# Performance work log

Hardware: AMD Instinct MI355X
Metric: run time of the kernel (lower is better)

The kernel has to match this reference:

```python
import jax, jax.numpy as jnp
import numpy as np

B, T, L, D, H = 4, 8, 197, 512, 8
DK = D // H
SIM_TH = 0.0
N = T * (L - 1)  # 1568 local tokens

def _ln(x, g, b, eps=1e-5):
    x32 = x.astype(jnp.float32)
    m = jnp.mean(x32, axis=-1, keepdims=True)
    v = jnp.mean((x32 - m) ** 2, axis=-1, keepdims=True)
    return (((x32 - m) * jax.lax.rsqrt(v + eps)) * g + b).astype(x.dtype)

def _qgelu(x):
    return x * jax.nn.sigmoid(1.702 * x)

def _mha(x, w_in, b_in, w_out, b_out):
    # torch nn.MultiheadAttention, x: [S, Bt, D] (seq-first)
    S, Bt, _ = x.shape
    qkv = x @ w_in.T + b_in
    q, k, v = jnp.split(qkv, 3, axis=-1)
    q = q.reshape(S, Bt, H, DK); k = k.reshape(S, Bt, H, DK); v = v.reshape(S, Bt, H, DK)
    scores = jnp.einsum('sbhd,tbhd->bhst', q, k) / jnp.sqrt(jnp.asarray(DK, x.dtype))
    p = jax.nn.softmax(scores, axis=-1)
    o = jnp.einsum('bhst,tbhd->sbhd', p, v).reshape(S, Bt, D)
    return o @ w_out.T + b_out

def _resblock(x, ln1g, ln1b, inw, inb, outw, outb, ln2g, ln2b, fcw, fcb, pw, pb):
    x = x + _mha(_ln(x, ln1g, ln1b), inw, inb, outw, outb)
    h = _qgelu(_ln(x, ln2g, ln2b) @ fcw.T + fcb)
    return x + h @ pw.T + pb

def _build_graph(x, g_mask):
    xd = jax.lax.stop_gradient(x)  # matches x.detach()
    xn = xd / jnp.maximum(jnp.linalg.norm(xd, axis=-1, keepdims=True), 1e-12)
    sim = jnp.einsum('bnd,bmd->bnm', xn, xn)
    adj = jnp.where(sim < SIM_TH, 0.0, sim)
    return adj * g_mask  # t != 1 branch

def _graph_attn(x, mask, wq, bq, wk, bk, wv, bv, wo, bo):
    Bb, Nn, _ = x.shape
    def heads(a):
        return a.reshape(Bb, Nn, H, DK).transpose(0, 2, 1, 3)
    Q = heads(x @ wq.T + bq); K = heads(x @ wk.T + bk); V = heads(x @ wv.T + bv)
    scores = jnp.einsum('bhnd,bhmd->bhnm', Q, K) / jnp.sqrt(jnp.asarray(DK, x.dtype))
    m = mask[:, None]  # [b,1,N,N]
    scores = jnp.where(m == 0, -jnp.inf, scores * m)  # scores*mask then masked_fill(mask==0,-inf)
    p = jax.nn.softmax(scores, axis=-1)
    o = jnp.einsum('bhnm,bhmd->bhnd', p, V).transpose(0, 2, 1, 3).reshape(Bb, Nn, D)
    return o @ wo.T + bo

def _forward(x, proj_w, proj_b,
             m_ln1g, m_ln1b, m_inw, m_inb, m_outw, m_outb,
             m_ln2g, m_ln2b, m_fcw, m_fcb, m_pw, m_pb,
             g_wq, g_bq, g_wk, g_bk, g_wv, g_bv, g_wo, g_bo,
             ln1g, ln1b, a_inw, a_inb, a_outw, a_outb,
             ln2g, ln2b, fcw, fcb, pw, pb, g_mask):
    b, t, l, d = x.shape
    x = x @ proj_w.T + proj_b
    glob = x[:, :, 0, :].transpose(1, 0, 2)  # [t,b,d]
    msg = (m_ln1g, m_ln1b, m_inw, m_inb, m_outw, m_outb, m_ln2g, m_ln2b, m_fcw, m_fcb, m_pw, m_pb)
    glob = _resblock(glob, *msg)
    glob = _resblock(glob, *msg)  # message_attn applied twice (shared weights)
    glob = glob.reshape(1, t, b, d)
    loc = x[:, :, 1:, :].reshape(b, t * (l - 1), d)
    gm = _build_graph(loc, g_mask)
    loc = _graph_attn(loc, gm, g_wq, g_bq, g_wk, g_bk, g_wv, g_bv, g_wo, g_bo)
    loc = loc.reshape(b, t, l - 1, d).transpose(2, 1, 0, 3)  # [l-1,t,b,d]
    y = jnp.concatenate([glob, loc], axis=0).reshape(l, t * b, d)
    y = y + _mha(_ln(y, ln1g, ln1b), a_inw, a_inb, a_outw, a_outb)
    y = y + _qgelu(_ln(y, ln2g, ln2b) @ fcw.T + fcb) @ pw.T + pb
    return y.reshape(l, t, b, d).transpose(2, 1, 0, 3)  # [b,t,l,d]

def setup_inputs() -> dict:
    key = jax.random.key(0)
    ks = jax.random.split(key, 64)
    s = 0.02
    def w(i, shape):
        return jax.random.normal(ks[i], shape, jnp.float32) * s
    ones = jnp.ones((D,), jnp.float32); zeros = jnp.zeros((D,), jnp.float32)
    gm = (jax.random.uniform(ks[60], (N, N)) < 0.5).astype(jnp.float32)
    gm = gm.at[jnp.arange(N), jnp.arange(N)].set(1.0)  # keep self-edges so no row is fully masked
    return dict(
        x=jax.random.normal(ks[0], (B, T, L, D), jnp.float32),
        proj_w=w(1, (D, D)), proj_b=jnp.zeros((D,), jnp.float32),
        m_ln1g=ones, m_ln1b=zeros,
        m_inw=w(2, (3 * D, D)), m_inb=jnp.zeros((3 * D,), jnp.float32),
        m_outw=w(3, (D, D)), m_outb=zeros,
        m_ln2g=ones, m_ln2b=zeros,
        m_fcw=w(4, (4 * D, D)), m_fcb=jnp.zeros((4 * D,), jnp.float32),
        m_pw=w(5, (D, 4 * D)), m_pb=zeros,
        g_wq=w(6, (D, D)), g_bq=zeros, g_wk=w(7, (D, D)), g_bk=zeros,
        g_wv=w(8, (D, D)), g_bv=zeros, g_wo=w(9, (D, D)), g_bo=zeros,
        ln1g=ones, ln1b=zeros,
        a_inw=w(10, (3 * D, D)), a_inb=jnp.zeros((3 * D,), jnp.float32),
        a_outw=w(11, (D, D)), a_outb=zeros,
        ln2g=ones, ln2b=zeros,
        fcw=w(12, (4 * D, D)), fcb=jnp.zeros((4 * D,), jnp.float32),
        pw=w(13, (D, 4 * D)), pb=zeros,
        g_mask=gm,
    )

def reference(x, proj_w, proj_b, m_ln1g, m_ln1b, m_inw, m_inb, m_outw, m_outb,
              m_ln2g, m_ln2b, m_fcw, m_fcb, m_pw, m_pb,
              g_wq, g_bq, g_wk, g_bk, g_wv, g_bv, g_wo, g_bo,
              ln1g, ln1b, a_inw, a_inb, a_outw, a_outb,
              ln2g, ln2b, fcw, fcb, pw, pb, g_mask):
    return _forward(x, proj_w, proj_b, m_ln1g, m_ln1b, m_inw, m_inb, m_outw, m_outb,
                    m_ln2g, m_ln2b, m_fcw, m_fcb, m_pw, m_pb,
                    g_wq, g_bq, g_wk, g_bk, g_wv, g_bv, g_wo, g_bo,
                    ln1g, ln1b, a_inw, a_inb, a_outw, a_outb,
                    ln2g, ln2b, fcw, fcb, pw, pb, g_mask)
```

## Files before the change

### kernel.cpp

```cpp
#include <hip/hip_runtime.h>
#include <hip/hip_bf16.h>

typedef unsigned short u16;
typedef __attribute__((ext_vector_type(8))) short bf16x8;
typedef __attribute__((ext_vector_type(4))) float f32x4;

#define FINF __builtin_huge_valf()

static __device__ __forceinline__ float bf2f(u16 v){ union{unsigned u; float f;} c; c.u = ((unsigned)v)<<16; return c.f; }
static __device__ __forceinline__ u16 f2bf(float f){ union{__hip_bfloat16 h; u16 u;} c; c.h = __float2bfloat16(f); return c.u; }

static __device__ __forceinline__ void gload16(const void* g, void* l){
  __builtin_amdgcn_global_load_lds(
      (const __attribute__((address_space(1))) void*)g,
      (__attribute__((address_space(3))) void*)l, 16, 0, 0);
}

struct CvtArgs {
  const float* src[14];
  u16* dst[14];
  int n[14];
};
__global__ __launch_bounds__(256) void cvt_multi(CvtArgs a){
  int seg = blockIdx.y;
  const float* s = a.src[seg]; u16* d = a.dst[seg]; int n = a.n[seg];
  for (int i = (blockIdx.x*256 + threadIdx.x)*4; i < n; i += gridDim.x*256*4){
    float4 v = *(const float4*)(s + i);
    ushort4 o = { f2bf(v.x), f2bf(v.y), f2bf(v.z), f2bf(v.w) };
    *(ushort4*)(d + i) = o;
  }
}

__global__ __launch_bounds__(256) void concat_bias(const float* a, const float* b, const float* c, float* o){
  int i = blockIdx.x*256 + threadIdx.x;
  o[i] = i < 512 ? a[i] : (i < 1024 ? b[i-512] : c[i-1024]);
}

template<int EPI>
__global__ __launch_bounds__(256,2) void gemm_nt(
    const u16* __restrict__ A, const u16* __restrict__ Bw,
    const float* __restrict__ bias, const float* aux, void* out,
    int M, int Nn, int K, int ldc, long aBatch, long bBatch, long cBatch)
{
  __shared__ __align__(16) u16 a_lds[8192];
  __shared__ __align__(16) u16 b_lds[8192];
  const int z = blockIdx.z;
  const u16* Az = A + (long)z*aBatch;
  const u16* Bz = Bw + (long)z*bBatch;
  const int n0 = blockIdx.x*128, m0 = blockIdx.y*128;
  const int t = threadIdx.x, lane = t & 63, wave = t >> 6;
  const int wr = wave >> 1, wc = wave & 1;
  const int r = lane & 15, kq = lane >> 4;

  const int srow = t >> 3;
  const int scol = ((((t&7)*16) ^ ((srow&7)<<4)) >> 1);
  int rowA[4], rowB[4];
  #pragma unroll
  for (int i=0;i<4;i++){
    int rloc = i*32 + srow;
    int ga = m0 + rloc; rowA[i] = ga < M ? ga : M-1;
    int gb = n0 + rloc; rowB[i] = gb < Nn ? gb : Nn-1;
  }

  f32x4 acc[4][4] = {};
  const int nkt = K >> 6;
  for (int kt=0; kt<nkt; kt++){
    const long koff = (long)kt*64 + scol;
    #pragma unroll
    for (int i=0;i<4;i++)
      gload16(Az + (long)rowA[i]*K + koff, (char*)a_lds + i*4096 + wave*1024);
    #pragma unroll
    for (int i=0;i<4;i++)
      gload16(Bz + (long)rowB[i]*K + koff, (char*)b_lds + i*4096 + wave*1024);
    __syncthreads();
    #pragma unroll
    for (int kk=0; kk<2; kk++){
      bf16x8 af[4], bfr[4];
      #pragma unroll
      for (int i=0;i<4;i++){
        int rw = wr*64 + i*16 + r;
        af[i] = *(const bf16x8*)&a_lds[rw*64 + ((kk*32 + kq*8) ^ ((rw&7)<<3))];
      }
      #pragma unroll
      for (int j=0;j<4;j++){
        int rw = wc*64 + j*16 + r;
        bfr[j] = *(const bf16x8*)&b_lds[rw*64 + ((kk*32 + kq*8) ^ ((rw&7)<<3))];
      }
      #pragma unroll
      for (int i=0;i<4;i++)
        #pragma unroll
        for (int j=0;j<4;j++)
          acc[i][j] = __builtin_amdgcn_mfma_f32_16x16x32_bf16(af[i], bfr[j], acc[i][j], 0,0,0);
    }
    __syncthreads();
  }

  #pragma unroll
  for (int i=0;i<4;i++){
    #pragma unroll
    for (int j=0;j<4;j++){
      int gcol = n0 + wc*64 + j*16 + r;
      if (gcol >= Nn) continue;
      float bv = bias ? bias[gcol] : 0.f;
      #pragma unroll
      for (int rr=0; rr<4; rr++){
        int grow = m0 + wr*64 + i*16 + kq*4 + rr;
        if (grow >= M) continue;
        float v = acc[i][j][rr] + bv;
        if constexpr (EPI==0){
          ((float*)out)[(long)z*cBatch + (long)grow*ldc + gcol] = v;
        } else if constexpr (EPI==1){
          ((u16*)out)[(long)z*cBatch + (long)grow*ldc + gcol] = f2bf(v);
        } else if constexpr (EPI==2){
          long idx = (long)z*cBatch + (long)grow*ldc + gcol;
          ((float*)out)[idx] = aux[idx] + v;
        } else if constexpr (EPI==3){
          float g = v / (1.f + __expf(-1.702f*v));
          ((u16*)out)[(long)z*cBatch + (long)grow*ldc + gcol] = f2bf(g);
        } else if constexpr (EPI==4){
          float adj = v < 0.f ? 0.f : v;
          float gmv = aux[(long)grow*Nn + gcol];
          ((u16*)out)[(long)z*cBatch + (long)grow*ldc + gcol] = f2bf(adj*gmv);
        } else if constexpr (EPI==5){
          int b = grow/1568, n = grow%1568, tt = n/196, lp = n%196;
          int yrow = (1+lp)*32 + tt*4 + b;
          ((float*)out)[(long)yrow*ldc + gcol] = v;
        }
      }
    }
  }
}

template<bool MASKED>
__global__ __launch_bounds__(256,2) void flash_attn(
    const u16* __restrict__ QKV, const u16* __restrict__ gmask, u16* __restrict__ Out,
    int nq, int nk, long qBatch, long qRow, long oBatch, long oRow, long gmBatch)
{
  __shared__ __align__(16) u16 k_lds[4096];
  __shared__ __align__(16) u16 g_lds[4096];
  __shared__ __align__(16) u16 vt[64*74];
  __shared__ u16 p_lds[4][16][72];
  const int h = blockIdx.y, z = blockIdx.z;
  const int t = threadIdx.x, lane = t&63, wave = t>>6;
  const int r = lane&15, kq = lane>>4;
  const u16* Qb = QKV + (long)z*qBatch + h*64;
  const u16* Kb = Qb + 512;
  const u16* Vb = Qb + 1024;
  const u16* Gz = gmask + (long)z*gmBatch;
  const int qt0 = blockIdx.x*64;
  const int q0 = qt0 + wave*16;

  bf16x8 qf0, qf1;
  {
    int qi = q0 + r; if (qi > nq-1) qi = nq-1;
    const u16* qp = Qb + (long)qi*qRow + kq*8;
    qf0 = *(const bf16x8*)qp;
    qf1 = *(const bf16x8*)(qp + 32);
  }

  const int srow = t>>3;
  const int scol = ((((t&7)*16) ^ ((srow&7)<<4)) >> 1);

  float m_[4] = {-FINF,-FINF,-FINF,-FINF};
  float l_[4] = {0,0,0,0};
  f32x4 o_[4] = {};

  const int nkt = (nk + 63) >> 6;
  for (int kt=0; kt<nkt; kt++){
    #pragma unroll
    for (int i=0;i<2;i++){
      int krow = i*32 + srow;
      int j = kt*64 + krow; if (j > nk-1) j = nk-1;
      gload16(Kb + (long)j*qRow + scol, (char*)k_lds + i*4096 + wave*1024);
    }
    if constexpr (MASKED){
      #pragma unroll
      for (int i=0;i<2;i++){
        int grow = i*32 + srow;
        int qr = qt0 + grow; if (qr > nq-1) qr = nq-1;
        gload16(Gz + (long)qr*nk + kt*64 + scol, (char*)g_lds + i*4096 + wave*1024);
      }
    }
    #pragma unroll
    for (int i=0;i<2;i++){
      int c = i*256 + t; int vrow = c>>3, cc = (c&7)*8;
      int vj = kt*64 + vrow; if (vj > nk-1) vj = nk-1;
      uint4 vv = *(const uint4*)(Vb + (long)vj*qRow + cc);
      #pragma unroll
      for (int e=0;e<8;e++) vt[(cc+e)*74 + vrow] = ((const u16*)&vv)[e];
    }
    __syncthreads();

    float s[4][4];
    #pragma unroll
    for (int sub=0; sub<4; sub++){
      int rw = sub*16 + r; int sw = (rw&7)<<3;
      bf16x8 kf0 = *(const bf16x8*)&k_lds[rw*64 + ((kq*8) ^ sw)];
      bf16x8 kf1 = *(const bf16x8*)&k_lds[rw*64 + ((32 + kq*8) ^ sw)];
      f32x4 sc = {};
      sc = __builtin_amdgcn_mfma_f32_16x16x32_bf16(qf0, kf0, sc, 0,0,0);
      sc = __builtin_amdgcn_mfma_f32_16x16x32_bf16(qf1, kf1, sc, 0,0,0);
      #pragma unroll
      for (int rr=0;rr<4;rr++) s[sub][rr] = sc[rr];
    }
    #pragma unroll
    for (int sub=0; sub<4; sub++){
      int key = kt*64 + sub*16 + r;
      bool kdead = key >= nk;
      #pragma unroll
      for (int rr=0;rr<4;rr++){
        float sv = s[sub][rr]*0.125f;
        if constexpr (MASKED){
          int lrow = wave*16 + kq*4 + rr;
          u16 g = g_lds[lrow*64 + ((sub*16+r) ^ ((lrow&7)<<3))];
          if (g == 0 || kdead) sv = -FINF; else sv *= bf2f(g);
        } else {
          if (kdead) sv = -FINF;
        }
        s[sub][rr] = sv;
      }
    }
    #pragma unroll
    for (int rr=0;rr<4;rr++){
      float mx = fmaxf(fmaxf(s[0][rr],s[1][rr]), fmaxf(s[2][rr],s[3][rr]));
      #pragma unroll
      for (int d=1; d<16; d<<=1) mx = fmaxf(mx, __shfl_xor(mx, d));
      float mnew = fmaxf(m_[rr], mx);
      float fac = (m_[rr] == -FINF) ? 0.f : __expf(m_[rr] - mnew);
      float ps = 0.f;
      #pragma unroll
      for (int sub=0;sub<4;sub++){
        float p = (s[sub][rr] == -FINF) ? 0.f : __expf(s[sub][rr] - mnew);
        s[sub][rr] = p; ps += p;
      }
      #pragma unroll
      for (int d=1; d<16; d<<=1) ps += __shfl_xor(ps, d);
      l_[rr] = l_[rr]*fac + ps;
      m_[rr] = mnew;
      o_[0][rr]*=fac; o_[1][rr]*=fac; o_[2][rr]*=fac; o_[3][rr]*=fac;
    }
    #pragma unroll
    for (int rr=0;rr<4;rr++){
      #pragma unroll
      for (int sub=0;sub<4;sub++)
        p_lds[wave][kq*4+rr][sub*16+r] = f2bf(s[sub][rr]);
    }
    #pragma unroll
    for (int c=0;c<2;c++){
      bf16x8 pf = *(const bf16x8*)&p_lds[wave][r][c*32 + kq*8];
      #pragma unroll
      for (int j=0;j<4;j++){
        bf16x8 vf = *(const bf16x8*)&vt[(j*16+r)*74 + c*32 + kq*8];
        o_[j] = __builtin_amdgcn_mfma_f32_16x16x32_bf16(pf, vf, o_[j], 0,0,0);
      }
    }
    __syncthreads();
  }

  #pragma unroll
  for (int rr=0;rr<4;rr++){
    int qrow = q0 + kq*4 + rr;
    if (qrow >= nq) continue;
    float inv = l_[rr] > 0.f ? 1.f/l_[rr] : 0.f;
    #pragma unroll
    for (int j=0;j<4;j++)
      Out[(long)z*oBatch + (long)qrow*oRow + h*64 + j*16 + r] = f2bf(o_[j][rr]*inv);
  }
}

__global__ __launch_bounds__(256) void ln_rows(const float* __restrict__ in,
    const float* __restrict__ g, const float* __restrict__ b, u16* __restrict__ out, int rows)
{
  int wave = threadIdx.x >> 6, lane = threadIdx.x & 63;
  int row = blockIdx.x*4 + wave;
  if (row >= rows) return;
  const float4* x = (const float4*)(in + (long)row*512);
  float4 v0 = x[lane], v1 = x[lane+64];
  float s  = v0.x+v0.y+v0.z+v0.w + v1.x+v1.y+v1.z+v1.w;
  float ss = v0.x*v0.x+v0.y*v0.y+v0.z*v0.z+v0.w*v0.w + v1.x*v1.x+v1.y*v1.y+v1.z*v1.z+v1.w*v1.w;
  #pragma unroll
  for (int d=1; d<64; d<<=1){ s += __shfl_xor(s,d); ss += __shfl_xor(ss,d); }
  float mean = s * (1.f/512.f);
  float var = ss * (1.f/512.f) - mean*mean;
  float rs = rsqrtf(var + 1e-5f);
  const float4* gg = (const float4*)g; const float4* bb = (const float4*)b;
  float4 g0 = gg[lane], g1 = gg[lane+64], b0 = bb[lane], b1 = bb[lane+64];
  u16* o = out + (long)row*512;
  ushort4 o0 = { f2bf((v0.x-mean)*rs*g0.x + b0.x), f2bf((v0.y-mean)*rs*g0.y + b0.y),
                 f2bf((v0.z-mean)*rs*g0.z + b0.z), f2bf((v0.w-mean)*rs*g0.w + b0.w) };
  ushort4 o1 = { f2bf((v1.x-mean)*rs*g1.x + b1.x), f2bf((v1.y-mean)*rs*g1.y + b1.y),
                 f2bf((v1.z-mean)*rs*g1.z + b1.z), f2bf((v1.w-mean)*rs*g1.w + b1.w) };
  *(ushort4*)(o + lane*4) = o0;
  *(ushort4*)(o + 256 + lane*4) = o1;
}

__global__ __launch_bounds__(256) void locprep(const float* __restrict__ y0,
    u16* __restrict__ xn, u16* __restrict__ locb)
{
  int wave = threadIdx.x >> 6, lane = threadIdx.x & 63;
  int rr = blockIdx.x*4 + wave;
  int bb = rr/1568, n = rr%1568, tt = n/196, lp = n%196;
  const float4* x = (const float4*)(y0 + ((long)((bb*8+tt)*197) + 1 + lp)*512);
  float4 v0 = x[lane], v1 = x[lane+64];
  float ss = v0.x*v0.x+v0.y*v0.y+v0.z*v0.z+v0.w*v0.w + v1.x*v1.x+v1.y*v1.y+v1.z*v1.z+v1.w*v1.w;
  #pragma unroll
  for (int d=1; d<64; d<<=1) ss += __shfl_xor(ss,d);
  float sc = 1.f / fmaxf(sqrtf(ss), 1e-12f);
  u16* ox = xn + (long)rr*512;
  u16* ol = locb + (long)rr*512;
  ushort4 a0 = { f2bf(v0.x*sc), f2bf(v0.y*sc), f2bf(v0.z*sc), f2bf(v0.w*sc) };
  ushort4 a1 = { f2bf(v1.x*sc), f2bf(v1.y*sc), f2bf(v1.z*sc), f2bf(v1.w*sc) };
  ushort4 c0 = { f2bf(v0.x), f2bf(v0.y), f2bf(v0.z), f2bf(v0.w) };
  ushort4 c1 = { f2bf(v1.x), f2bf(v1.y), f2bf(v1.z), f2bf(v1.w) };
  *(ushort4*)(ox + lane*4) = a0;  *(ushort4*)(ox + 256 + lane*4) = a1;
  *(ushort4*)(ol + lane*4) = c0;  *(ushort4*)(ol + 256 + lane*4) = c1;
}

__global__ __launch_bounds__(64) void msg_attn(const u16* __restrict__ mqkv, u16* __restrict__ matt){
  __shared__ float q_s[8][64], k_s[8][64], v_s[8][64];
  int bh = blockIdx.x; int bt = bh>>3, h = bh&7;
  int lane = threadIdx.x;
  int row = lane>>3, cc = (lane&7)*8;
  #pragma unroll
  for (int e=0;e<8;e++){
    long base = (long)(row*4 + bt)*1536 + h*64 + cc + e;
    q_s[row][cc+e] = bf2f(mqkv[base]);
    k_s[row][cc+e] = bf2f(mqkv[base + 512]);
    v_s[row][cc+e] = bf2f(mqkv[base + 1024]);
  }
  __syncthreads();
  int q = lane>>3, k = lane&7;
  float s = 0.f;
  #pragma unroll 16
  for (int d=0; d<64; d++) s += q_s[q][d]*k_s[k][d];
  s *= 0.125f;
  float mx = s;
  #pragma unroll
  for (int d=1; d<8; d<<=1) mx = fmaxf(mx, __shfl_xor(mx,d));
  float p = __expf(s - mx), ps = p;
  #pragma unroll
  for (int d=1; d<8; d<<=1) ps += __shfl_xor(ps,d);
  p /= ps;
  for (int d=0; d<64; d++){
    float ov = p * v_s[k][d];
    #pragma unroll
    for (int m=1; m<8; m<<=1) ov += __shfl_xor(ov,m);
    if (k == (d>>3)) matt[(long)(q*4 + bt)*512 + h*64 + d] = f2bf(ov);
  }
}

__global__ __launch_bounds__(256) void gather_glob(const float* __restrict__ y0, float* __restrict__ glob){
  int idx = blockIdx.x*256 + threadIdx.x;
  int orow = idx>>9, d = idx&511;
  int tt = orow>>2, bb = orow&3;
  glob[idx] = y0[((long)(bb*8+tt)*197)*512 + d];
}
__global__ __launch_bounds__(256) void copy32(const float* __restrict__ glob, float* __restrict__ y){
  int idx = blockIdx.x*256 + threadIdx.x;
  y[idx] = glob[idx];
}
__global__ __launch_bounds__(256) void permute_out(const float* __restrict__ y, float* __restrict__ out){
  int idx = blockIdx.x*256 + threadIdx.x;
  int d4 = idx & 127;
  int rest = idx >> 7;
  int l = rest % 197;
  int bt = rest / 197;
  int tt = bt & 7, bb = bt >> 3;
  ((float4*)out)[idx] = ((const float4*)y)[(l*32 + tt*4 + bb)*128 + d4];
}

extern "C" void kernel_launch(void* const* d_in, const int* in_sizes, int n_in,
                              void* d_out, int out_size, void* d_ws, size_t ws_size,
                              hipStream_t stream)
{
  const float* x      = (const float*)d_in[0];
  const float* proj_w = (const float*)d_in[1];
  const float* proj_b = (const float*)d_in[2];
  const float* m_ln1g = (const float*)d_in[3];
  const float* m_ln1b = (const float*)d_in[4];
  const float* m_inw  = (const float*)d_in[5];
  const float* m_inb  = (const float*)d_in[6];
  const float* m_outw = (const float*)d_in[7];
  const float* m_outb = (const float*)d_in[8];
  const float* m_ln2g = (const float*)d_in[9];
  const float* m_ln2b = (const float*)d_in[10];
  const float* m_fcw  = (const float*)d_in[11];
  const float* m_fcb  = (const float*)d_in[12];
  const float* m_pw   = (const float*)d_in[13];
  const float* m_pb   = (const float*)d_in[14];
  const float* g_wq = (const float*)d_in[15]; const float* g_bq = (const float*)d_in[16];
  const float* g_wk = (const float*)d_in[17]; const float* g_bk = (const float*)d_in[18];
  const float* g_wv = (const float*)d_in[19]; const float* g_bv = (const float*)d_in[20];
  const float* g_wo = (const float*)d_in[21]; const float* g_bo = (const float*)d_in[22];
  const float* ln1g = (const float*)d_in[23]; const float* ln1b = (const float*)d_in[24];
  const float* a_inw = (const float*)d_in[25]; const float* a_inb = (const float*)d_in[26];
  const float* a_outw = (const float*)d_in[27]; const float* a_outb = (const float*)d_in[28];
  const float* ln2g = (const float*)d_in[29]; const float* ln2b = (const float*)d_in[30];
  const float* fcw = (const float*)d_in[31]; const float* fcb = (const float*)d_in[32];
  const float* pw = (const float*)d_in[33]; const float* pb = (const float*)d_in[34];
  const float* g_mask = (const float*)d_in[35];

  if (ws_size < (size_t)99753984) return;

  char* ws = (char*)d_ws;
  u16* WB = (u16*)ws;
  const long WPROJ=0, WMIN=262144, WMOUT=1048576, WMFC=1310720, WMP=2359296,
             WGQ=3407872, WGK=3670016, WGV=3932160, WGO=4194304,
             WAIN=4456448, WAOUT=5242880, WFC=5505024, WP=6553600;
  float* y0   = (float*)(ws + 15204352);
  float* y    = (float*)(ws + 28114944);
  u16* lnbuf  = (u16*)(ws + 41025536);
  u16* locb   = (u16*)(ws + 47480832);
  u16* qkv    = (u16*)(ws + 53903360);
  u16* xb     = (u16*)(ws + 73269248);
  u16* gm     = (u16*)(ws + 73269248);
  u16* hbuf   = (u16*)(ws + 73269248);
  u16* obuf   = (u16*)(ws + 92938240);
  float* glob = (float*)(ws + 99393536);
  u16* mlnb   = (u16*)(ws + 99459072);
  u16* mqkv   = (u16*)(ws + 99491840);
  u16* matt   = (u16*)(ws + 99590144);
  u16* mh     = (u16*)(ws + 99622912);
  float* gbias = (float*)(ws + 99622912);

  CvtArgs ca;
  auto setseg=[&](int i, const float* s, u16* d, int n){ ca.src[i]=s; ca.dst[i]=d; ca.n[i]=n; };
  setseg(0,  x,      xb,       6304*512);
  setseg(1,  proj_w, WB+WPROJ, 262144);
  setseg(2,  m_inw,  WB+WMIN,  786432);
  setseg(3,  m_outw, WB+WMOUT, 262144);
  setseg(4,  m_fcw,  WB+WMFC,  1048576);
  setseg(5,  m_pw,   WB+WMP,   1048576);
  setseg(6,  g_wq,   WB+WGQ,   262144);
  setseg(7,  g_wk,   WB+WGK,   262144);
  setseg(8,  g_wv,   WB+WGV,   262144);
  setseg(9,  g_wo,   WB+WGO,   262144);
  setseg(10, a_inw,  WB+WAIN,  786432);
  setseg(11, a_outw, WB+WAOUT, 262144);
  setseg(12, fcw,    WB+WFC,   1048576);
  setseg(13, pw,     WB+WP,    1048576);
  cvt_multi<<<dim3(128,14), 256, 0, stream>>>(ca);

  gemm_nt<0><<<dim3(4,50), 256, 0, stream>>>(xb, WB+WPROJ, proj_b, nullptr, y0, 6304,512,512,512, 0,0,0);

  gather_glob<<<64,256,0,stream>>>(y0, glob);

  for (int it=0; it<2; ++it){
    ln_rows<<<8,256,0,stream>>>(glob, m_ln1g, m_ln1b, mlnb, 32);
    gemm_nt<1><<<dim3(12,1),256,0,stream>>>(mlnb, WB+WMIN, m_inb, nullptr, mqkv, 32,1536,512,1536, 0,0,0);
    msg_attn<<<32,64,0,stream>>>(mqkv, matt);
    gemm_nt<2><<<dim3(4,1),256,0,stream>>>(matt, WB+WMOUT, m_outb, glob, glob, 32,512,512,512, 0,0,0);
    ln_rows<<<8,256,0,stream>>>(glob, m_ln2g, m_ln2b, mlnb, 32);
    gemm_nt<3><<<dim3(16,1),256,0,stream>>>(mlnb, WB+WMFC, m_fcb, nullptr, mh, 32,2048,512,2048, 0,0,0);
    gemm_nt<2><<<dim3(4,1),256,0,stream>>>(mh, WB+WMP, m_pb, glob, glob, 32,512,2048,512, 0,0,0);
  }

  concat_bias<<<6,256,0,stream>>>(g_bq, g_bk, g_bv, gbias);

  locprep<<<1568,256,0,stream>>>(y0, lnbuf, locb);

  gemm_nt<4><<<dim3(13,13,4),256,0,stream>>>(lnbuf, lnbuf, nullptr, g_mask, gm,
      1568,1568,512,1568, 1568L*512, 1568L*512, 1568L*1568);

  gemm_nt<1><<<dim3(12,49),256,0,stream>>>(locb, WB+WGQ, gbias, nullptr, qkv, 6272,1536,512,1536, 0,0,0);

  flash_attn<true><<<dim3(25,8,4),256,0,stream>>>(qkv, gm, obuf,
      1568,1568, 1568L*1536, 1536, 1568L*512, 512, 1568L*1568);

  gemm_nt<5><<<dim3(4,49),256,0,stream>>>(obuf, WB+WGO, g_bo, nullptr, y, 6272,512,512,512, 0,0,0);

  copy32<<<64,256,0,stream>>>(glob, y);

  ln_rows<<<1576,256,0,stream>>>(y, ln1g, ln1b, lnbuf, 6304);
  gemm_nt<1><<<dim3(12,50),256,0,stream>>>(lnbuf, WB+WAIN, a_inb, nullptr, qkv, 6304,1536,512,1536, 0,0,0);
  flash_attn<false><<<dim3(4,8,32),256,0,stream>>>(qkv, nullptr, obuf,
      197,197, 1536, 32L*1536, 512, 32L*512, 0);
  gemm_nt<2><<<dim3(4,50),256,0,stream>>>(obuf, WB+WAOUT, a_outb, y, y, 6304,512,512,512, 0,0,0);

  ln_rows<<<1576,256,0,stream>>>(y, ln2g, ln2b, lnbuf, 6304);
  gemm_nt<3><<<dim3(16,50),256,0,stream>>>(lnbuf, WB+WFC, fcb, nullptr, hbuf, 6304,2048,512,2048, 0,0,0);
  gemm_nt<2><<<dim3(4,50),256,0,stream>>>(hbuf, WB+WP, pb, y, y, 6304,512,2048,512, 0,0,0);

  permute_out<<<3153,256,0,stream>>>(y, (float*)d_out);
}
```

Baseline: 629.7 us.

## Double-buffer GEMM and flash-attention LDS tiles, add 64-row tiles, fuse output permute

The GEMM main loop now double-buffers its A/B LDS tiles and prefetches the next k-tile while the MFMAs run, replacing two __syncthreads per iteration with one explicit vmcnt wait and barrier. A BM template parameter lets the narrow N=512 GEMMs use 64-row tiles, giving about twice as many blocks. The flash-attention kernel double-buffers K, V and a transposed mask tile through registers and LDS, and swizzles the P scratch buffer to cut bank conflicts. The last projection GEMM writes straight into the permuted output layout, so the permute_out kernel goes away. Doubling the LDS buffers may reduce occupancy, and the hand-written waitcnt and barrier placement has to be exactly right to avoid races.

```diff
diff --git a/kernel.cpp b/kernel.cpp
--- a/kernel.cpp
+++ b/kernel.cpp
@@ -15,6 +15,10 @@
       (const __attribute__((address_space(1))) void*)g,
       (__attribute__((address_space(3))) void*)l, 16, 0, 0);
 }
+
+#define WAIT_VM0()   { asm volatile("s_waitcnt vmcnt(0)" ::: "memory"); __builtin_amdgcn_sched_barrier(0); }
+#define WAIT_LGKM0() { asm volatile("s_waitcnt lgkmcnt(0)" ::: "memory"); __builtin_amdgcn_sched_barrier(0); }
+#define BARRIER()    { __builtin_amdgcn_sched_barrier(0); __builtin_amdgcn_s_barrier(); __builtin_amdgcn_sched_barrier(0); }
 
 struct CvtArgs {
   const float* src[14];
@@ -36,67 +40,76 @@
   o[i] = i < 512 ? a[i] : (i < 1024 ? b[i-512] : c[i-1024]);
 }
 
-template<int EPI>
+template<int BM, int EPI>
 __global__ __launch_bounds__(256,2) void gemm_nt(
     const u16* __restrict__ A, const u16* __restrict__ Bw,
     const float* __restrict__ bias, const float* aux, void* out,
     int M, int Nn, int K, int ldc, long aBatch, long bBatch, long cBatch)
 {
-  __shared__ __align__(16) u16 a_lds[8192];
-  __shared__ __align__(16) u16 b_lds[8192];
+  constexpr int MI = BM/32;
+  constexpr int WSPAN = BM/2;
+  __shared__ __align__(16) u16 a_lds[2*BM*64];
+  __shared__ __align__(16) u16 b_lds[2*128*64];
   const int z = blockIdx.z;
   const u16* Az = A + (long)z*aBatch;
   const u16* Bz = Bw + (long)z*bBatch;
-  const int n0 = blockIdx.x*128, m0 = blockIdx.y*128;
+  const int n0 = blockIdx.x*128, m0 = blockIdx.y*BM;
   const int t = threadIdx.x, lane = t & 63, wave = t >> 6;
   const int wr = wave >> 1, wc = wave & 1;
   const int r = lane & 15, kq = lane >> 4;
 
   const int srow = t >> 3;
-  const int scol = ((((t&7)*16) ^ ((srow&7)<<4)) >> 1);
-  int rowA[4], rowB[4];
-  #pragma unroll
-  for (int i=0;i<4;i++){
-    int rloc = i*32 + srow;
-    int ga = m0 + rloc; rowA[i] = ga < M ? ga : M-1;
-    int gb = n0 + rloc; rowB[i] = gb < Nn ? gb : Nn-1;
-  }
-
-  f32x4 acc[4][4] = {};
+  const int scol = ((t&7)*8) ^ ((srow&7)<<3);
+  int rowA[MI], rowB[4];
+  #pragma unroll
+  for (int i=0;i<MI;i++){ int ga = m0 + i*32 + srow; rowA[i] = ga < M ? ga : M-1; }
+  #pragma unroll
+  for (int i=0;i<4;i++){ int gb = n0 + i*32 + srow; rowB[i] = gb < Nn ? gb : Nn-1; }
+
+  f32x4 acc[MI][4] = {};
   const int nkt = K >> 6;
+
+  auto STAGE = [&](int kt, int buf){
+    const long koff = (long)kt*64 + scol;
+    #pragma unroll
+    for (int i=0;i<MI;i++)
+      gload16(Az + (long)rowA[i]*K + koff, (char*)a_lds + buf*(BM*128) + i*4096 + wave*1024);
+    #pragma unroll
+    for (int i=0;i<4;i++)
+      gload16(Bz + (long)rowB[i]*K + koff, (char*)b_lds + buf*16384 + i*4096 + wave*1024);
+  };
+
+  STAGE(0,0);
+  WAIT_VM0(); BARRIER();
   for (int kt=0; kt<nkt; kt++){
-    const long koff = (long)kt*64 + scol;
-    #pragma unroll
-    for (int i=0;i<4;i++)
-      gload16(Az + (long)rowA[i]*K + koff, (char*)a_lds + i*4096 + wave*1024);
-    #pragma unroll
-    for (int i=0;i<4;i++)
-      gload16(Bz + (long)rowB[i]*K + koff, (char*)b_lds + i*4096 + wave*1024);
-    __syncthreads();
+    const int cur = kt&1;
+    if (kt+1 < nkt) STAGE(kt+1, cur^1);
+    const u16* al = a_lds + cur*BM*64;
+    const u16* bl = b_lds + cur*8192;
     #pragma unroll
     for (int kk=0; kk<2; kk++){
-      bf16x8 af[4], bfr[4];
-      #pragma unroll
-      for (int i=0;i<4;i++){
-        int rw = wr*64 + i*16 + r;
-        af[i] = *(const bf16x8*)&a_lds[rw*64 + ((kk*32 + kq*8) ^ ((rw&7)<<3))];
+      bf16x8 af[MI], bfr[4];
+      #pragma unroll
+      for (int i=0;i<MI;i++){
+        int rw = wr*WSPAN + i*16 + r;
+        af[i] = *(const bf16x8*)&al[rw*64 + ((kk*32 + kq*8) ^ ((rw&7)<<3))];
       }
       #pragma unroll
       for (int j=0;j<4;j++){
         int rw = wc*64 + j*16 + r;
-        bfr[j] = *(const bf16x8*)&b_lds[rw*64 + ((kk*32 + kq*8) ^ ((rw&7)<<3))];
+        bfr[j] = *(const bf16x8*)&bl[rw*64 + ((kk*32 + kq*8) ^ ((rw&7)<<3))];
       }
       #pragma unroll
-      for (int i=0;i<4;i++)
+      for (int i=0;i<MI;i++)
         #pragma unroll
         for (int j=0;j<4;j++)
           acc[i][j] = __builtin_amdgcn_mfma_f32_16x16x32_bf16(af[i], bfr[j], acc[i][j], 0,0,0);
     }
-    __syncthreads();
-  }
-
-  #pragma unroll
-  for (int i=0;i<4;i++){
+    WAIT_VM0(); BARRIER();
+  }
+
+  #pragma unroll
+  for (int i=0;i<MI;i++){
     #pragma unroll
     for (int j=0;j<4;j++){
       int gcol = n0 + wc*64 + j*16 + r;
@@ -104,7 +117,7 @@
       float bv = bias ? bias[gcol] : 0.f;
       #pragma unroll
       for (int rr=0; rr<4; rr++){
-        int grow = m0 + wr*64 + i*16 + kq*4 + rr;
+        int grow = m0 + wr*WSPAN + i*16 + kq*4 + rr;
         if (grow >= M) continue;
         float v = acc[i][j][rr] + bv;
         if constexpr (EPI==0){
@@ -125,6 +138,10 @@
           int b = grow/1568, n = grow%1568, tt = n/196, lp = n%196;
           int yrow = (1+lp)*32 + tt*4 + b;
           ((float*)out)[(long)yrow*ldc + gcol] = v;
+        } else if constexpr (EPI==6){
+          long idx = (long)grow*ldc + gcol;
+          int l = grow>>5, rb = grow&31, tt = rb>>2, bb = rb&3;
+          ((float*)out)[((long)((bb*8+tt)*197) + l)*512 + gcol] = aux[idx] + v;
         }
       }
     }
@@ -136,10 +153,10 @@
     const u16* __restrict__ QKV, const u16* __restrict__ gmask, u16* __restrict__ Out,
     int nq, int nk, long qBatch, long qRow, long oBatch, long oRow, long gmBatch)
 {
-  __shared__ __align__(16) u16 k_lds[4096];
-  __shared__ __align__(16) u16 g_lds[4096];
-  __shared__ __align__(16) u16 vt[64*74];
-  __shared__ u16 p_lds[4][16][72];
+  __shared__ __align__(16) u16 k_lds[2][4096];
+  __shared__ __align__(16) u16 vt[2][64*74];
+  __shared__ __align__(16) u16 gt[MASKED?2:1][MASKED?64*70:4];
+  __shared__ __align__(16) u16 p_lds[4][16*72];
   const int h = blockIdx.y, z = blockIdx.z;
   const int t = threadIdx.x, lane = t&63, wave = t>>6;
   const int r = lane&15, kq = lane>>4;
@@ -159,44 +176,74 @@
   }
 
   const int srow = t>>3;
-  const int scol = ((((t&7)*16) ^ ((srow&7)<<4)) >> 1);
+  const int scol = ((t&7)*8) ^ ((srow&7)<<3);
+
+  uint4 vv[2]; uint4 gv[2];
+
+  auto stage_k = [&](int kt, int buf){
+    #pragma unroll
+    for (int i=0;i<2;i++){
+      int j = kt*64 + i*32 + srow; if (j > nk-1) j = nk-1;
+      gload16(Kb + (long)j*qRow + scol, (char*)&k_lds[buf][0] + i*4096 + wave*1024);
+    }
+  };
+  auto load_v = [&](int kt){
+    #pragma unroll
+    for (int i=0;i<2;i++){
+      int c = i*256 + t; int vj = kt*64 + (c>>3); if (vj > nk-1) vj = nk-1;
+      vv[i] = *(const uint4*)(Vb + (long)vj*qRow + (c&7)*8);
+    }
+  };
+  auto load_g = [&](int kt){
+    #pragma unroll
+    for (int i=0;i<2;i++){
+      int c = i*256 + t; int qr = qt0 + (c>>3); if (qr > nq-1) qr = nq-1;
+      gv[i] = *(const uint4*)(Gz + (long)qr*nk + kt*64 + (c&7)*8);
+    }
+  };
+  auto write_vt = [&](int buf){
+    #pragma unroll
+    for (int i=0;i<2;i++){
+      int c = i*256 + t; int vrow = c>>3, cc = (c&7)*8;
+      #pragma unroll
+      for (int e=0;e<8;e++) vt[buf][(cc+e)*74 + vrow] = ((const u16*)&vv[i])[e];
+    }
+  };
+  auto write_gt = [&](int buf){
+    #pragma unroll
+    for (int i=0;i<2;i++){
+      int c = i*256 + t; int qlr = c>>3, cc = (c&7)*8;
+      #pragma unroll
+      for (int e=0;e<8;e++) gt[buf][(cc+e)*70 + qlr] = ((const u16*)&gv[i])[e];
+    }
+  };
 
   float m_[4] = {-FINF,-FINF,-FINF,-FINF};
   float l_[4] = {0,0,0,0};
   f32x4 o_[4] = {};
 
   const int nkt = (nk + 63) >> 6;
+  stage_k(0,0); load_v(0);
+  if constexpr (MASKED) load_g(0);
+  WAIT_VM0(); BARRIER();
+
   for (int kt=0; kt<nkt; kt++){
-    #pragma unroll
-    for (int i=0;i<2;i++){
-      int krow = i*32 + srow;
-      int j = kt*64 + krow; if (j > nk-1) j = nk-1;
-      gload16(Kb + (long)j*qRow + scol, (char*)k_lds + i*4096 + wave*1024);
-    }
-    if constexpr (MASKED){
-      #pragma unroll
-      for (int i=0;i<2;i++){
-        int grow = i*32 + srow;
-        int qr = qt0 + grow; if (qr > nq-1) qr = nq-1;
-        gload16(Gz + (long)qr*nk + kt*64 + scol, (char*)g_lds + i*4096 + wave*1024);
-      }
-    }
-    #pragma unroll
-    for (int i=0;i<2;i++){
-      int c = i*256 + t; int vrow = c>>3, cc = (c&7)*8;
-      int vj = kt*64 + vrow; if (vj > nk-1) vj = nk-1;
-      uint4 vv = *(const uint4*)(Vb + (long)vj*qRow + cc);
-      #pragma unroll
-      for (int e=0;e<8;e++) vt[(cc+e)*74 + vrow] = ((const u16*)&vv)[e];
-    }
-    __syncthreads();
+    const int cur = kt&1;
+    write_vt(cur);
+    if constexpr (MASKED) write_gt(cur);
+    if (kt+1 < nkt){
+      stage_k(kt+1, cur^1);
+      load_v(kt+1);
+      if constexpr (MASKED) load_g(kt+1);
+    }
+    WAIT_LGKM0(); BARRIER();
 
     float s[4][4];
     #pragma unroll
     for (int sub=0; sub<4; sub++){
       int rw = sub*16 + r; int sw = (rw&7)<<3;
-      bf16x8 kf0 = *(const bf16x8*)&k_lds[rw*64 + ((kq*8) ^ sw)];
-      bf16x8 kf1 = *(const bf16x8*)&k_lds[rw*64 + ((32 + kq*8) ^ sw)];
+      bf16x8 kf0 = *(const bf16x8*)&k_lds[cur][rw*64 + ((kq*8) ^ sw)];
+      bf16x8 kf1 = *(const bf16x8*)&k_lds[cur][rw*64 + ((32 + kq*8) ^ sw)];
       f32x4 sc = {};
       sc = __builtin_amdgcn_mfma_f32_16x16x32_bf16(qf0, kf0, sc, 0,0,0);
       sc = __builtin_amdgcn_mfma_f32_16x16x32_bf16(qf1, kf1, sc, 0,0,0);
@@ -212,7 +259,7 @@
         float sv = s[sub][rr]*0.125f;
         if constexpr (MASKED){
           int lrow = wave*16 + kq*4 + rr;
-          u16 g = g_lds[lrow*64 + ((sub*16+r) ^ ((lrow&7)<<3))];
+          u16 g = gt[cur][(sub*16+r)*70 + lrow];
           if (g == 0 || kdead) sv = -FINF; else sv *= bf2f(g);
         } else {
           if (kdead) sv = -FINF;
@@ -241,20 +288,21 @@
     }
     #pragma unroll
     for (int rr=0;rr<4;rr++){
+      int prow = kq*4+rr;
       #pragma unroll
       for (int sub=0;sub<4;sub++)
-        p_lds[wave][kq*4+rr][sub*16+r] = f2bf(s[sub][rr]);
+        p_lds[wave][prow*72 + ((sub*16+r) ^ ((prow&7)<<3))] = f2bf(s[sub][rr]);
     }
     #pragma unroll
     for (int c=0;c<2;c++){
-      bf16x8 pf = *(const bf16x8*)&p_lds[wave][r][c*32 + kq*8];
+      bf16x8 pf = *(const bf16x8*)&p_lds[wave][r*72 + ((c*32 + kq*8) ^ ((r&7)<<3))];
       #pragma unroll
       for (int j=0;j<4;j++){
-        bf16x8 vf = *(const bf16x8*)&vt[(j*16+r)*74 + c*32 + kq*8];
+        bf16x8 vf = *(const bf16x8*)&vt[cur][(j*16+r)*74 + c*32 + kq*8];
         o_[j] = __builtin_amdgcn_mfma_f32_16x16x32_bf16(pf, vf, o_[j], 0,0,0);
       }
     }
-    __syncthreads();
+    WAIT_VM0(); BARRIER();
   }
 
   #pragma unroll
@@ -358,15 +406,6 @@
 __global__ __launch_bounds__(256) void copy32(const float* __restrict__ glob, float* __restrict__ y){
   int idx = blockIdx.x*256 + threadIdx.x;
   y[idx] = glob[idx];
-}
-__global__ __launch_bounds__(256) void permute_out(const float* __restrict__ y, float* __restrict__ out){
-  int idx = blockIdx.x*256 + threadIdx.x;
-  int d4 = idx & 127;
-  int rest = idx >> 7;
-  int l = rest % 197;
-  int bt = rest / 197;
-  int tt = bt & 7, bb = bt >> 3;
-  ((float4*)out)[idx] = ((const float4*)y)[(l*32 + tt*4 + bb)*128 + d4];
 }
 
 extern "C" void kernel_launch(void* const* d_in, const int* in_sizes, int n_in,
@@ -441,45 +480,43 @@
   setseg(13, pw,     WB+WP,    1048576);
   cvt_multi<<<dim3(128,14), 256, 0, stream>>>(ca);
 
-  gemm_nt<0><<<dim3(4,50), 256, 0, stream>>>(xb, WB+WPROJ, proj_b, nullptr, y0, 6304,512,512,512, 0,0,0);
+  gemm_nt<64,0><<<dim3(4,99), 256, 0, stream>>>(xb, WB+WPROJ, proj_b, nullptr, y0, 6304,512,512,512, 0,0,0);
 
   gather_glob<<<64,256,0,stream>>>(y0, glob);
 
   for (int it=0; it<2; ++it){
     ln_rows<<<8,256,0,stream>>>(glob, m_ln1g, m_ln1b, mlnb, 32);
-    gemm_nt<1><<<dim3(12,1),256,0,stream>>>(mlnb, WB+WMIN, m_inb, nullptr, mqkv, 32,1536,512,1536, 0,0,0);
+    gemm_nt<64,1><<<dim3(12,1),256,0,stream>>>(mlnb, WB+WMIN, m_inb, nullptr, mqkv, 32,1536,512,1536, 0,0,0);
     msg_attn<<<32,64,0,stream>>>(mqkv, matt);
-    gemm_nt<2><<<dim3(4,1),256,0,stream>>>(matt, WB+WMOUT, m_outb, glob, glob, 32,512,512,512, 0,0,0);
+    gemm_nt<64,2><<<dim3(4,1),256,0,stream>>>(matt, WB+WMOUT, m_outb, glob, glob, 32,512,512,512, 0,0,0);
     ln_rows<<<8,256,0,stream>>>(glob, m_ln2g, m_ln2b, mlnb, 32);
-    gemm_nt<3><<<dim3(16,1),256,0,stream>>>(mlnb, WB+WMFC, m_fcb, nullptr, mh, 32,2048,512,2048, 0,0,0);
-    gemm_nt<2><<<dim3(4,1),256,0,stream>>>(mh, WB+WMP, m_pb, glob, glob, 32,512,2048,512, 0,0,0);
+    gemm_nt<64,3><<<dim3(16,1),256,0,stream>>>(mlnb, WB+WMFC, m_fcb, nullptr, mh, 32,2048,512,2048, 0,0,0);
+    gemm_nt<64,2><<<dim3(4,1),256,0,stream>>>(mh, WB+WMP, m_pb, glob, glob, 32,512,2048,512, 0,0,0);
   }
 
   concat_bias<<<6,256,0,stream>>>(g_bq, g_bk, g_bv, gbias);
 
   locprep<<<1568,256,0,stream>>>(y0, lnbuf, locb);
 
-  gemm_nt<4><<<dim3(13,13,4),256,0,stream>>>(lnbuf, lnbuf, nullptr, g_mask, gm,
+  gemm_nt<128,4><<<dim3(13,13,4),256,0,stream>>>(lnbuf, lnbuf, nullptr, g_mask, gm,
       1568,1568,512,1568, 1568L*512, 1568L*512, 1568L*1568);
 
-  gemm_nt<1><<<dim3(12,49),256,0,stream>>>(locb, WB+WGQ, gbias, nullptr, qkv, 6272,1536,512,1536, 0,0,0);
+  gemm_nt<128,1><<<dim3(12,49),256,0,stream>>>(locb, WB+WGQ, gbias, nullptr, qkv, 6272,1536,512,1536, 0,0,0);
 
   flash_attn<true><<<dim3(25,8,4),256,0,stream>>>(qkv, gm, obuf,
       1568,1568, 1568L*1536, 1536, 1568L*512, 512, 1568L*1568);
 
-  gemm_nt<5><<<dim3(4,49),256,0,stream>>>(obuf, WB+WGO, g_bo, nullptr, y, 6272,512,512,512, 0,0,0);
+  gemm_nt<64,5><<<dim3(4,98),256,0,stream>>>(obuf, WB+WGO, g_bo, nullptr, y, 6272,512,512,512, 0,0,0);
 
   copy32<<<64,256,0,stream>>>(glob, y);
 
   ln_rows<<<1576,256,0,stream>>>(y, ln1g, ln1b, lnbuf, 6304);
-  gemm_nt<1><<<dim3(12,50),256,0,stream>>>(lnbuf, WB+WAIN, a_inb, nullptr, qkv, 6304,1536,512,1536, 0,0,0);
+  gemm_nt<128,1><<<dim3(12,50),256,0,stream>>>(lnbuf, WB+WAIN, a_inb, nullptr, qkv, 6304,1536,512,1536, 0,0,0);
   flash_attn<false><<<dim3(4,8,32),256,0,stream>>>(qkv, nullptr, obuf,
       197,197, 1536, 32L*1536, 512, 32L*512, 0);
-  gemm_nt<2><<<dim3(4,50),256,0,stream>>>(obuf, WB+WAOUT, a_outb, y, y, 6304,512,512,512, 0,0,0);
+  gemm_nt<64,2><<<dim3(4,99),256,0,stream>>>(obuf, WB+WAOUT, a_outb, y, y, 6304,512,512,512, 0,0,0);
 
   ln_rows<<<1576,256,0,stream>>>(y, ln2g, ln2b, lnbuf, 6304);
-  gemm_nt<3><<<dim3(16,50),256,0,stream>>>(lnbuf, WB+WFC, fcb, nullptr, hbuf, 6304,2048,512,2048, 0,0,0);
-  gemm_nt<2><<<dim3(4,50),256,0,stream>>>(hbuf, WB+WP, pb, y, y, 6304,512,2048,512, 0,0,0);
-
-  permute_out<<<3153,256,0,stream>>>(y, (float*)d_out);
-}
+  gemm_nt<128,3><<<dim3(16,50),256,0,stream>>>(lnbuf, WB+WFC, fcb, nullptr, hbuf, 6304,2048,512,2048, 0,0,0);
+  gemm_nt<64,6><<<dim3(4,99),256,0,stream>>>(hbuf, WB+WP, pb, y, (float*)d_out, 6304,512,2048,512, 0,0,0);
+}
```

After: 649.7 us. 3.2% more time.
